# Kernel optimization log

Hardware: AMD Instinct MI355X
Metric: run time of the kernel (lower is better)

Reference implementation:

```python
import jax, jax.numpy as jnp
import numpy as np

N = 200_000          # active voxels
C = 64               # in/out channels
K = 3                # kernel size per dim
SHAPE = (128, 128, 128)  # spatial grid (D, H, W)
B = 2                # batch size
KV = K ** 3          # 27 kernel offsets


def setup_inputs() -> dict:
    key = jax.random.key(0)
    kb, kz, ky, kx, kf, k0, k1 = jax.random.split(key, 7)
    b = jax.random.randint(kb, (N, 1), 0, B, dtype=jnp.int32)
    z = jax.random.randint(kz, (N, 1), 0, SHAPE[0], dtype=jnp.int32)
    y = jax.random.randint(ky, (N, 1), 0, SHAPE[1], dtype=jnp.int32)
    x = jax.random.randint(kx, (N, 1), 0, SHAPE[2], dtype=jnp.int32)
    coors = jnp.concatenate([b, z, y, x], axis=1)  # [N, 4] (batch, z, y, x)
    features = jax.random.normal(kf, (N, C), dtype=jnp.float32)
    W0 = jax.random.normal(k0, (KV, C, C), dtype=jnp.float32) * 0.05  # layer 0 weights per offset
    W1 = jax.random.normal(k1, (KV, C, C), dtype=jnp.float32) * 0.05  # layer 1 weights per offset
    return {"features": features, "coors": coors, "W0": W0, "W1": W1, "batch_size": B}


def _neighbor_indices(coors, batch_size):
    """Rulebook: for each of the 27 kernel offsets, index of the active input
    voxel feeding each active output voxel, or -1 if that neighbor is inactive."""
    D, H, W = SHAPE
    n = coors.shape[0]
    # dense coord -> row-index hash grid
    flat = ((coors[:, 0] * D + coors[:, 1]) * H + coors[:, 2]) * W + coors[:, 3]
    grid = jnp.full((batch_size * D * H * W,), -1, dtype=jnp.int32)
    grid = grid.at[flat].set(jnp.arange(n, dtype=jnp.int32))
    r = K // 2
    ax = jnp.arange(-r, r + 1, dtype=jnp.int32)
    offs = jnp.stack(jnp.meshgrid(ax, ax, ax, indexing="ij"), axis=-1).reshape(-1, 3)  # [27, 3]
    shp = jnp.array(SHAPE, dtype=jnp.int32)
    nb_coord = coors[None, :, 1:] + offs[:, None, :]               # [27, N, 3]
    valid = jnp.all((nb_coord >= 0) & (nb_coord < shp), axis=-1)   # [27, N]
    nc = jnp.clip(nb_coord, 0, shp - 1)
    nflat = ((coors[None, :, 0] * D + nc[..., 0]) * H + nc[..., 1]) * W + nc[..., 2]
    nb = grid[nflat]                                               # [27, N]
    return jnp.where(valid, nb, -1)


def _subm_conv(feats, W, nb):
    # gather -> per-offset GEMM -> accumulate (all offsets fused in one einsum)
    mask = (nb >= 0)
    g = feats[jnp.maximum(nb, 0)] * mask[..., None].astype(feats.dtype)  # [27, N, C]
    return jnp.einsum("knc,kco->no", g, W)  # [N, C]


def reference(features, coors, W0, W1, batch_size):
    coors = coors.astype(jnp.int32)
    nb = _neighbor_indices(coors, batch_size)  # active set is preserved across subm layers
    x = _subm_conv(features, W0, nb)
    return _subm_conv(x, W1, nb)
```

## Files before the change

### kernel.cpp

```cpp
#include <hip/hip_runtime.h>
#include <stdint.h>

#define SD 128
#define SH 128
#define SW 128
#define BATCH 2
#define CCH 64
#define KV 27
#define NCELL (BATCH * SD * SH * SW)
#define CHUNK 4096
#define NCHUNK (NCELL / CHUNK)

typedef __attribute__((ext_vector_type(4))) float f32x4;
typedef __attribute__((ext_vector_type(8))) short s16x8;

__device__ __forceinline__ unsigned short f2bf_rne(float f) {
    union { float f; unsigned int u; } v; v.f = f;
    unsigned int u = v.u;
    return (unsigned short)((u + 0x7FFFu + ((u >> 16) & 1u)) >> 16);
}

__device__ __forceinline__ s16x8 pack_bf8(float4 a, float4 b) {
    s16x8 o;
    o[0] = (short)f2bf_rne(a.x); o[1] = (short)f2bf_rne(a.y);
    o[2] = (short)f2bf_rne(a.z); o[3] = (short)f2bf_rne(a.w);
    o[4] = (short)f2bf_rne(b.x); o[5] = (short)f2bf_rne(b.y);
    o[6] = (short)f2bf_rne(b.z); o[7] = (short)f2bf_rne(b.w);
    return o;
}


__global__ void k_wprep(const float* __restrict__ W, unsigned short* __restrict__ Wt) {
    int idx = blockIdx.x * blockDim.x + threadIdx.x;
    if (idx >= KV * CCH * CCH) return;
    int k = idx / (CCH * CCH);
    int rem = idx - k * CCH * CCH;
    int ci = rem >> 6, co = rem & 63;
    int d = ((k * 8 + (ci >> 3)) * 64 + co) * 8 + (ci & 7);
    Wt[d] = f2bf_rne(W[idx]);
}

__global__ void k_scatter(const int4* __restrict__ coors, int* __restrict__ grid, int n) {
    int i = blockIdx.x * blockDim.x + threadIdx.x;
    if (i >= n) return;
    int4 c = coors[i];
    int flat = ((c.x * SD + c.y) * SH + c.z) * SW + c.w;
    atomicMax(&grid[flat], i);
}


__global__ void k_count(const int4* __restrict__ grid4, int* __restrict__ counts) {
    int t = threadIdx.x;
    size_t base = (size_t)blockIdx.x * (CHUNK / 4) + t * 4;
    int cnt = 0;
#pragma unroll
    for (int i = 0; i < 4; ++i) {
        int4 v = grid4[base + i];
        cnt += (v.x >= 0) + (v.y >= 0) + (v.z >= 0) + (v.w >= 0);
    }
    __shared__ int s[256];
    s[t] = cnt; __syncthreads();
    for (int d = 128; d > 0; d >>= 1) {
        if (t < d) s[t] += s[t + d];
        __syncthreads();
    }
    if (t == 0) counts[blockIdx.x] = s[0];
}

__global__ void k_scan(const int* __restrict__ counts, int* __restrict__ excl, int* __restrict__ ctr) {
    int t = threadIdx.x, lane = t & 63, w = t >> 6;
    int v = counts[t];
    int s = v;
#pragma unroll
    for (int d = 1; d < 64; d <<= 1) {
        int u = __shfl_up(s, d);
        if (lane >= d) s += u;
    }
    __shared__ int wsum[16];
    if (lane == 63) wsum[w] = s;
    __syncthreads();
    if (w == 0 && lane < 16) {
        int x = wsum[lane];
#pragma unroll
        for (int d = 1; d < 16; d <<= 1) {
            int u = __shfl_up(x, d);
            if (lane >= d) x += u;
        }
        wsum[lane] = x;
    }
    __syncthreads();
    int add = (w > 0) ? wsum[w - 1] : 0;
    excl[t] = add + s - v;
    if (t == 1023) ctr[0] = add + s;
}

__global__ void k_compact(int* __restrict__ grid, const int* __restrict__ excl,
                          int* __restrict__ perm) {
    int t = threadIdx.x;
    size_t cellbase = (size_t)blockIdx.x * CHUNK + t * 16;
    int v[16];
    const int4* g4 = (const int4*)(grid + cellbase);
#pragma unroll
    for (int i = 0; i < 4; ++i) {
        int4 a = g4[i];
        v[i * 4 + 0] = a.x; v[i * 4 + 1] = a.y; v[i * 4 + 2] = a.z; v[i * 4 + 3] = a.w;
    }
    int cnt = 0;
#pragma unroll
    for (int i = 0; i < 16; ++i) cnt += (v[i] >= 0);
    __shared__ int s[256];
    s[t] = cnt; __syncthreads();
    for (int d = 1; d < 256; d <<= 1) {
        int a = (t >= d) ? s[t - d] : 0;
        __syncthreads();
        s[t] += a;
        __syncthreads();
    }
    int idx = excl[blockIdx.x] + s[t] - cnt;
#pragma unroll
    for (int i = 0; i < 16; ++i) {
        if (v[i] >= 0) {
            perm[idx] = v[i];
            grid[cellbase + i] = idx;
            idx++;
        }
    }
}

__global__ void k_losers(const int4* __restrict__ coors, const int* __restrict__ grid,
                         int* __restrict__ perm, int* __restrict__ ctr, int n) {
    int j = blockIdx.x * blockDim.x + threadIdx.x;
    if (j >= n) return;
    int4 c = coors[j];
    int flat = ((c.x * SD + c.y) * SH + c.z) * SW + c.w;
    int si = grid[flat];
    if (perm[si] != j) {
        int s = atomicAdd(ctr, 1);
        perm[s] = j;
    }
}

__global__ void k_permfeat(const float4* __restrict__ feats4, const int4* __restrict__ coors,
                           const int* __restrict__ perm, s16x8* __restrict__ fs,
                           int* __restrict__ fb, int n) {
    int tid = blockIdx.x * blockDim.x + threadIdx.x;
    int i = tid >> 3, j = tid & 7;
    if (i >= n) return;
    int src = perm[i];
    float4 p0 = feats4[(size_t)src * 16 + j * 2];
    float4 p1 = feats4[(size_t)src * 16 + j * 2 + 1];
    fs[(size_t)i * 8 + j] = pack_bf8(p0, p1);
    if (j == 0) {
        int4 c = coors[src];
        fb[i] = ((c.x * SD + c.y) * SH + c.z) * SW + c.w;
    }
}

template <int OUT_PERM>
__global__ __launch_bounds__(256) void k_conv_s(const s16x8* __restrict__ fin,
                                                const s16x8* __restrict__ wt,
                                                const int* __restrict__ fb,
                                                const int* __restrict__ grid,
                                                const int* __restrict__ perm,
                                                void* __restrict__ outp, int n) {
    __shared__ s16x8 wbuf[2][512];

    int nwg = gridDim.x, orig = blockIdx.x;
    int q = nwg >> 3, rr = nwg & 7;
    int xcd = orig & 7, bidx = orig >> 3;
    int blk = (xcd < rr ? xcd * (q + 1) : rr * (q + 1) + (xcd - rr) * q) + bidx;

    int tid = threadIdx.x;
    int w = tid >> 6, lane = tid & 63;
    int wid = blk * 4 + w;
    int base = wid * 32;
    int r = lane & 15;
    int g = lane >> 4;
    int li = lane & 31;
    int myrow = base + li;
    int rowok = (myrow < n) ? 1 : 0;
    int fbv = fb[rowok ? myrow : 0];
    int pl = 0;
    if (OUT_PERM) pl = rowok ? perm[myrow] : 0;
    int z = (fbv >> 14) & 127, y = (fbv >> 7) & 127, x = fbv & 127;

    f32x4 acc[2][4] = {};

    auto lookup = [&](int k) -> int {
        int dz = k / 9 - 1, dy = (k / 3) % 3 - 1, dx = k % 3 - 1;
        int zz = z + dz, yy = y + dy, xx = x + dx;
        int v = -1;
        if (rowok && (unsigned)zz < SD && (unsigned)yy < SH && (unsigned)xx < SW)
            v = grid[fbv + dz * (SH * SW) + dy * SW + dx];
        return v;
    };

    {
        s16x8 s0 = wt[tid];
        s16x8 s1 = wt[256 + tid];
        wbuf[0][tid] = s0;
        wbuf[0][256 + tid] = s1;
    }
    __syncthreads();

    int nbr = lookup(0);
    for (int k = 0; k < KV; ++k) {
        int kn = (k + 1 < KV) ? k + 1 : KV - 1;
        s16x8 st0 = wt[(size_t)kn * 512 + tid];
        s16x8 st1 = wt[(size_t)kn * 512 + 256 + tid];

        int nbr_next = (k + 1 < KV) ? lookup(k + 1) : -1;
        int nb0 = __shfl(nbr, r);
        int nb1 = __shfl(nbr, 16 + r);
        nbr = nbr_next;
        unsigned long long m0 = __ballot(nb0 >= 0);
        unsigned long long m1 = __ballot(nb1 >= 0);

        if (m0 | m1) {
            const s16x8* wb = &wbuf[k & 1][0];
            s16x8 bf[2][4];
#pragma unroll
            for (int s = 0; s < 2; ++s)
#pragma unroll
                for (int t = 0; t < 4; ++t)
                    bf[s][t] = wb[(s * 4 + g) * 64 + t * 16 + r];

            int nbh[2] = {nb0, nb1};
            unsigned long long mm[2] = {m0, m1};
#pragma unroll
            for (int h = 0; h < 2; ++h) {
                if (!mm[h]) continue;
                int nbx = nbh[h];
                s16x8 a0 = {}, a1 = {};
                if (nbx >= 0) {
                    a0 = fin[(size_t)nbx * 8 + g];
                    a1 = fin[(size_t)nbx * 8 + 4 + g];
                }
#pragma unroll
                for (int t = 0; t < 4; ++t) {
                    acc[h][t] = __builtin_amdgcn_mfma_f32_16x16x32_bf16(a0, bf[0][t], acc[h][t], 0, 0, 0);
                    acc[h][t] = __builtin_amdgcn_mfma_f32_16x16x32_bf16(a1, bf[1][t], acc[h][t], 0, 0, 0);
                }
            }
        }

        wbuf[(k + 1) & 1][tid] = st0;
        wbuf[(k + 1) & 1][256 + tid] = st1;
        __syncthreads();
    }

    if (OUT_PERM) {
        float* __restrict__ o = (float*)outp;
#pragma unroll
        for (int h = 0; h < 2; ++h)
#pragma unroll
            for (int t = 0; t < 4; ++t)
#pragma unroll
                for (int j = 0; j < 4; ++j) {
                    int ww = h * 16 + g * 4 + j;
                    if (base + ww < n) {
                        int orow = __shfl(pl, ww);
                        o[(size_t)orow * 64 + t * 16 + r] = acc[h][t][j];
                    }
                }
    } else {
        unsigned short* __restrict__ o = (unsigned short*)outp;
#pragma unroll
        for (int h = 0; h < 2; ++h)
#pragma unroll
            for (int t = 0; t < 4; ++t)
#pragma unroll
                for (int j = 0; j < 4; ++j) {
                    int row = base + h * 16 + g * 4 + j;
                    if (row < n) o[(size_t)row * 64 + t * 16 + r] = f2bf_rne(acc[h][t][j]);
                }
    }
}

extern "C" void kernel_launch(void* const* d_in, const int* in_sizes, int n_in,
                              void* d_out, int out_size, void* d_ws, size_t ws_size,
                              hipStream_t stream) {
    const float* feats = (const float*)d_in[0];
    const int4* coors = (const int4*)d_in[1];
    const float* W0 = (const float*)d_in[2];
    const float* W1 = (const float*)d_in[3];
    int N = in_sizes[0] / CCH;

    char* p = (char*)d_ws;
    auto carve = [&](size_t bytes) -> char* {
        char* q = p;
        p += (bytes + 255) & ~(size_t)255;
        return q;
    };

    size_t grid_bytes = (size_t)NCELL * 4;
    int* grid = (int*)carve(grid_bytes);
    unsigned short* wt0 = (unsigned short*)carve((size_t)KV * CCH * CCH * 2);
    unsigned short* wt1 = (unsigned short*)carve((size_t)KV * CCH * CCH * 2);
    int* counts = (int*)carve(NCHUNK * 4);
    int* excl = (int*)carve(NCHUNK * 4);
    int* ctr = (int*)carve(256);
    int* perm = (int*)carve((size_t)N * 4);
    int* fb = (int*)carve((size_t)N * 4);
    s16x8* fs = (s16x8*)carve((size_t)N * CCH * 2);
    s16x8* ibf_s = (s16x8*)carve((size_t)N * CCH * 2);

    int nw = KV * CCH * CCH;
    int tiles = (N + 31) / 32;
    int blocks = (tiles + 3) / 4;

    hipMemsetAsync(grid, 0xFF, grid_bytes, stream);
    k_wprep<<<(nw + 255) / 256, 256, 0, stream>>>(W0, wt0);
    k_wprep<<<(nw + 255) / 256, 256, 0, stream>>>(W1, wt1);
    k_scatter<<<(N + 255) / 256, 256, 0, stream>>>(coors, grid, N);
    k_count<<<NCHUNK, 256, 0, stream>>>((const int4*)grid, counts);
    k_scan<<<1, 1024, 0, stream>>>(counts, excl, ctr);
    k_compact<<<NCHUNK, 256, 0, stream>>>(grid, excl, perm);
    k_losers<<<(N + 255) / 256, 256, 0, stream>>>(coors, grid, perm, ctr, N);
    k_permfeat<<<((N * 8) + 255) / 256, 256, 0, stream>>>((const float4*)feats, coors, perm, fs, fb, N);
    k_conv_s<0><<<blocks, 256, 0, stream>>>(fs, (const s16x8*)wt0, fb, grid, perm, ibf_s, N);
    k_conv_s<1><<<blocks, 256, 0, stream>>>(ibf_s, (const s16x8*)wt1, fb, grid, perm, d_out, N);
}
```

Measured before the change: 298.8 us.

## Prefetch neighbor features one offset ahead and fold scan into compaction

The conv kernel now loads the gathered feature fragments for offset k+1 and looks up the neighbor index for k+2 while issuing MFMAs for offset k. This hides gather latency behind compute. The separate scan kernel is removed: each compact block sums all preceding chunk counts itself. The two weight-prep launches are merged into one. The extra prefetch raises register pressure. The per-block prefix sum re-reads up to 1024 counts per block, which is redundant work in exchange for one fewer launch.

```diff
diff --git a/kernel.cpp b/kernel.cpp
--- a/kernel.cpp
+++ b/kernel.cpp
@@ -10,6 +10,7 @@
 #define NCELL (BATCH * SD * SH * SW)
 #define CHUNK 4096
 #define NCHUNK (NCELL / CHUNK)
+#define NWELEM (KV * CCH * CCH)
 
 typedef __attribute__((ext_vector_type(4))) float f32x4;
 typedef __attribute__((ext_vector_type(8))) short s16x8;
@@ -30,14 +31,19 @@
 }
 
 
-__global__ void k_wprep(const float* __restrict__ W, unsigned short* __restrict__ Wt) {
+__global__ void k_wprep2(const float* __restrict__ W0, const float* __restrict__ W1,
+                         unsigned short* __restrict__ Wt0, unsigned short* __restrict__ Wt1) {
     int idx = blockIdx.x * blockDim.x + threadIdx.x;
-    if (idx >= KV * CCH * CCH) return;
-    int k = idx / (CCH * CCH);
-    int rem = idx - k * CCH * CCH;
+    if (idx >= 2 * NWELEM) return;
+    int which = idx >= NWELEM;
+    int id = idx - which * NWELEM;
+    const float* W = which ? W1 : W0;
+    unsigned short* Wt = which ? Wt1 : Wt0;
+    int k = id / (CCH * CCH);
+    int rem = id - k * CCH * CCH;
     int ci = rem >> 6, co = rem & 63;
     int d = ((k * 8 + (ci >> 3)) * 64 + co) * 8 + (ci & 7);
-    Wt[d] = f2bf_rne(W[idx]);
+    Wt[d] = f2bf_rne(W[id]);
 }
 
 __global__ void k_scatter(const int4* __restrict__ coors, int* __restrict__ grid, int n) {
@@ -67,37 +73,21 @@
     if (t == 0) counts[blockIdx.x] = s[0];
 }
 
-__global__ void k_scan(const int* __restrict__ counts, int* __restrict__ excl, int* __restrict__ ctr) {
-    int t = threadIdx.x, lane = t & 63, w = t >> 6;
-    int v = counts[t];
-    int s = v;
-#pragma unroll
-    for (int d = 1; d < 64; d <<= 1) {
-        int u = __shfl_up(s, d);
-        if (lane >= d) s += u;
-    }
-    __shared__ int wsum[16];
-    if (lane == 63) wsum[w] = s;
+__global__ void k_compact(int* __restrict__ grid, const int* __restrict__ counts,
+                          int* __restrict__ perm, int* __restrict__ ctr) {
+    int t = threadIdx.x, b = blockIdx.x;
+    __shared__ int s[256];
+    int part = 0;
+    for (int j = t; j < b; j += 256) part += counts[j];
+    s[t] = part; __syncthreads();
+    for (int d = 128; d > 0; d >>= 1) {
+        if (t < d) s[t] += s[t + d];
+        __syncthreads();
+    }
+    int exclv = s[0];
     __syncthreads();
-    if (w == 0 && lane < 16) {
-        int x = wsum[lane];
-#pragma unroll
-        for (int d = 1; d < 16; d <<= 1) {
-            int u = __shfl_up(x, d);
-            if (lane >= d) x += u;
-        }
-        wsum[lane] = x;
-    }
-    __syncthreads();
-    int add = (w > 0) ? wsum[w - 1] : 0;
-    excl[t] = add + s - v;
-    if (t == 1023) ctr[0] = add + s;
-}
-
-__global__ void k_compact(int* __restrict__ grid, const int* __restrict__ excl,
-                          int* __restrict__ perm) {
-    int t = threadIdx.x;
-    size_t cellbase = (size_t)blockIdx.x * CHUNK + t * 16;
+
+    size_t cellbase = (size_t)b * CHUNK + t * 16;
     int v[16];
     const int4* g4 = (const int4*)(grid + cellbase);
 #pragma unroll
@@ -108,7 +98,6 @@
     int cnt = 0;
 #pragma unroll
     for (int i = 0; i < 16; ++i) cnt += (v[i] >= 0);
-    __shared__ int s[256];
     s[t] = cnt; __syncthreads();
     for (int d = 1; d < 256; d <<= 1) {
         int a = (t >= d) ? s[t - d] : 0;
@@ -116,7 +105,7 @@
         s[t] += a;
         __syncthreads();
     }
-    int idx = excl[blockIdx.x] + s[t] - cnt;
+    int idx = exclv + s[t] - cnt;
 #pragma unroll
     for (int i = 0; i < 16; ++i) {
         if (v[i] >= 0) {
@@ -125,6 +114,7 @@
             idx++;
         }
     }
+    if (b == NCHUNK - 1 && t == 255) ctr[0] = exclv + s[255];
 }
 
 __global__ void k_losers(const int4* __restrict__ coors, const int* __restrict__ grid,
@@ -195,58 +185,67 @@
         return v;
     };
 
+    wbuf[0][tid] = wt[tid];
+    wbuf[0][256 + tid] = wt[256 + tid];
+
+    int nbrB;
+    unsigned long long m0c, m1c;
+    s16x8 ca00 = {}, ca01 = {}, ca10 = {}, ca11 = {};
     {
-        s16x8 s0 = wt[tid];
-        s16x8 s1 = wt[256 + tid];
-        wbuf[0][tid] = s0;
-        wbuf[0][256 + tid] = s1;
+        int nbrA = lookup(0);
+        nbrB = lookup(1);
+        int nb0 = __shfl(nbrA, r), nb1 = __shfl(nbrA, 16 + r);
+        m0c = __ballot(nb0 >= 0);
+        m1c = __ballot(nb1 >= 0);
+        if (nb0 >= 0) { ca00 = fin[(size_t)nb0 * 8 + g]; ca01 = fin[(size_t)nb0 * 8 + 4 + g]; }
+        if (nb1 >= 0) { ca10 = fin[(size_t)nb1 * 8 + g]; ca11 = fin[(size_t)nb1 * 8 + 4 + g]; }
     }
     __syncthreads();
 
-    int nbr = lookup(0);
     for (int k = 0; k < KV; ++k) {
+        s16x8 bf[2][4];
+        const s16x8* wb = &wbuf[k & 1][0];
+#pragma unroll
+        for (int s = 0; s < 2; ++s)
+#pragma unroll
+            for (int t = 0; t < 4; ++t)
+                bf[s][t] = wb[(s * 4 + g) * 64 + t * 16 + r];
+
         int kn = (k + 1 < KV) ? k + 1 : KV - 1;
         s16x8 st0 = wt[(size_t)kn * 512 + tid];
         s16x8 st1 = wt[(size_t)kn * 512 + 256 + tid];
 
-        int nbr_next = (k + 1 < KV) ? lookup(k + 1) : -1;
-        int nb0 = __shfl(nbr, r);
-        int nb1 = __shfl(nbr, 16 + r);
-        nbr = nbr_next;
-        unsigned long long m0 = __ballot(nb0 >= 0);
-        unsigned long long m1 = __ballot(nb1 >= 0);
-
-        if (m0 | m1) {
-            const s16x8* wb = &wbuf[k & 1][0];
-            s16x8 bf[2][4];
-#pragma unroll
-            for (int s = 0; s < 2; ++s)
-#pragma unroll
-                for (int t = 0; t < 4; ++t)
-                    bf[s][t] = wb[(s * 4 + g) * 64 + t * 16 + r];
-
-            int nbh[2] = {nb0, nb1};
-            unsigned long long mm[2] = {m0, m1};
-#pragma unroll
-            for (int h = 0; h < 2; ++h) {
-                if (!mm[h]) continue;
-                int nbx = nbh[h];
-                s16x8 a0 = {}, a1 = {};
-                if (nbx >= 0) {
-                    a0 = fin[(size_t)nbx * 8 + g];
-                    a1 = fin[(size_t)nbx * 8 + 4 + g];
-                }
-#pragma unroll
-                for (int t = 0; t < 4; ++t) {
-                    acc[h][t] = __builtin_amdgcn_mfma_f32_16x16x32_bf16(a0, bf[0][t], acc[h][t], 0, 0, 0);
-                    acc[h][t] = __builtin_amdgcn_mfma_f32_16x16x32_bf16(a1, bf[1][t], acc[h][t], 0, 0, 0);
-                }
+        int nbrC = (k + 2 < KV) ? lookup(k + 2) : -1;
+
+        int nb0n = __shfl(nbrB, r), nb1n = __shfl(nbrB, 16 + r);
+        unsigned long long m0n = __ballot(nb0n >= 0);
+        unsigned long long m1n = __ballot(nb1n >= 0);
+        s16x8 na00 = {}, na01 = {}, na10 = {}, na11 = {};
+        if (nb0n >= 0) { na00 = fin[(size_t)nb0n * 8 + g]; na01 = fin[(size_t)nb0n * 8 + 4 + g]; }
+        if (nb1n >= 0) { na10 = fin[(size_t)nb1n * 8 + g]; na11 = fin[(size_t)nb1n * 8 + 4 + g]; }
+
+        if (m0c) {
+#pragma unroll
+            for (int t = 0; t < 4; ++t) {
+                acc[0][t] = __builtin_amdgcn_mfma_f32_16x16x32_bf16(ca00, bf[0][t], acc[0][t], 0, 0, 0);
+                acc[0][t] = __builtin_amdgcn_mfma_f32_16x16x32_bf16(ca01, bf[1][t], acc[0][t], 0, 0, 0);
             }
         }
+        if (m1c) {
+#pragma unroll
+            for (int t = 0; t < 4; ++t) {
+                acc[1][t] = __builtin_amdgcn_mfma_f32_16x16x32_bf16(ca10, bf[0][t], acc[1][t], 0, 0, 0);
+                acc[1][t] = __builtin_amdgcn_mfma_f32_16x16x32_bf16(ca11, bf[1][t], acc[1][t], 0, 0, 0);
+            }
+        }
 
         wbuf[(k + 1) & 1][tid] = st0;
         wbuf[(k + 1) & 1][256 + tid] = st1;
         __syncthreads();
+
+        nbrB = nbrC;
+        ca00 = na00; ca01 = na01; ca10 = na10; ca11 = na11;
+        m0c = m0n; m1c = m1n;
     }
 
     if (OUT_PERM) {
@@ -295,27 +294,23 @@
 
     size_t grid_bytes = (size_t)NCELL * 4;
     int* grid = (int*)carve(grid_bytes);
-    unsigned short* wt0 = (unsigned short*)carve((size_t)KV * CCH * CCH * 2);
-    unsigned short* wt1 = (unsigned short*)carve((size_t)KV * CCH * CCH * 2);
+    unsigned short* wt0 = (unsigned short*)carve((size_t)NWELEM * 2);
+    unsigned short* wt1 = (unsigned short*)carve((size_t)NWELEM * 2);
     int* counts = (int*)carve(NCHUNK * 4);
-    int* excl = (int*)carve(NCHUNK * 4);
     int* ctr = (int*)carve(256);
     int* perm = (int*)carve((size_t)N * 4);
     int* fb = (int*)carve((size_t)N * 4);
     s16x8* fs = (s16x8*)carve((size_t)N * CCH * 2);
     s16x8* ibf_s = (s16x8*)carve((size_t)N * CCH * 2);
 
-    int nw = KV * CCH * CCH;
     int tiles = (N + 31) / 32;
     int blocks = (tiles + 3) / 4;
 
     hipMemsetAsync(grid, 0xFF, grid_bytes, stream);
-    k_wprep<<<(nw + 255) / 256, 256, 0, stream>>>(W0, wt0);
-    k_wprep<<<(nw + 255) / 256, 256, 0, stream>>>(W1, wt1);
+    k_wprep2<<<(2 * NWELEM + 255) / 256, 256, 0, stream>>>(W0, W1, wt0, wt1);
     k_scatter<<<(N + 255) / 256, 256, 0, stream>>>(coors, grid, N);
     k_count<<<NCHUNK, 256, 0, stream>>>((const int4*)grid, counts);
-    k_scan<<<1, 1024, 0, stream>>>(counts, excl, ctr);
-    k_compact<<<NCHUNK, 256, 0, stream>>>(grid, excl, perm);
+    k_compact<<<NCHUNK, 256, 0, stream>>>(grid, counts, perm, ctr);
     k_losers<<<(N + 255) / 256, 256, 0, stream>>>(coors, grid, perm, ctr, N);
     k_permfeat<<<((N * 8) + 255) / 256, 256, 0, stream>>>((const float4*)feats, coors, perm, fs, fb, N);
     k_conv_s<0><<<blocks, 256, 0, stream>>>(fs, (const s16x8*)wt0, fb, grid, perm, ibf_s, N);
```

Measured after the change: 296.4 us. Within noise of the previous version (-0.8%).
